# Optimization experiments

Hardware: AMD Instinct MI355X
Metric: run time of the kernel (lower is better)

The kernel has to match this reference:

```python
import jax, jax.numpy as jnp
import numpy as np

GAMMA = 1.0


def setup_inputs() -> dict:
    key = jax.random.key(0)
    kx, ky = jax.random.split(key)
    x = jax.random.normal(kx, (8192, 128), dtype=jnp.float32)
    y = jax.random.normal(ky, (8192, 128), dtype=jnp.float32)
    return {"x": x, "y": y}


def reference(x, y):
    # RBF kernel K[i,j] = exp(-gamma * ||x_i - y_j||^2)
    x2 = jnp.sum(x * x, axis=1)              # [N]
    y2 = jnp.sum(y * y, axis=1)              # [M]
    xy = jnp.einsum('nd,md->nm', x, y)       # [N, M] GEMM
    sq = x2[:, None] + y2[None, :] - 2.0 * xy
    sq = jnp.maximum(sq, 0.0)                # guard tiny negatives from cancellation
    return jnp.exp(-GAMMA * sq)
```

## Files before the change

### kernel.cpp

```cpp
#include <hip/hip_runtime.h>
#include <hip/hip_bf16.h>

typedef __bf16 bf16x8 __attribute__((ext_vector_type(8)));
typedef float f32x4 __attribute__((ext_vector_type(4)));
typedef unsigned short us4 __attribute__((ext_vector_type(4)));

__device__ __forceinline__ unsigned short f2bf(float f) {
    unsigned u = __float_as_uint(f);
    u += 0x7fffu + ((u >> 16) & 1u);
    return (unsigned short)(u >> 16);
}

__global__ __launch_bounds__(256)
void rbf_prep(const float* __restrict__ X, const float* __restrict__ Y,
              unsigned short* __restrict__ Xb, unsigned short* __restrict__ Yb,
              float* __restrict__ x2, float* __restrict__ y2) {
    const int b = blockIdx.x;
    const float* src = (b < 128) ? X : Y;
    unsigned short* db = (b < 128) ? Xb : Yb;
    float* dn = (b < 128) ? x2 : y2;
    const int r0 = (b & 127) * 64;
    const int t = threadIdx.x;
    const f32x4* s4 = (const f32x4*)(src + (size_t)r0 * 128);
#pragma unroll
    for (int i = 0; i < 8; ++i) {
        int idx = i * 256 + t;
        int r = idx >> 5, c4 = idx & 31;
        f32x4 v = s4[idx];
        us4 o;
        o.x = f2bf(v[0]); o.y = f2bf(v[1]); o.z = f2bf(v[2]); o.w = f2bf(v[3]);
        int pc = (c4 >> 1) ^ (r & 7);
        *(us4*)&db[(size_t)(r0 + r) * 128 + pc * 8 + (c4 & 1) * 4] = o;
    }
    if (t < 64) {
        const f32x4* row = (const f32x4*)(src + (size_t)(r0 + t) * 128);
        float s = 0.f;
#pragma unroll
        for (int c = 0; c < 32; ++c) {
            f32x4 v = row[c];
            s += v[0] * v[0] + v[1] * v[1] + v[2] * v[2] + v[3] * v[3];
        }
        dn[r0 + t] = s;
    }
}

__global__ __launch_bounds__(256, 2)
void rbf_main(const unsigned short* __restrict__ Xb, const unsigned short* __restrict__ Yb,
              const float* __restrict__ x2, const float* __restrict__ y2,
              float* __restrict__ O, int ldo) {
    __shared__ __align__(16) unsigned short Ab[16384];
    __shared__ __align__(16) unsigned short Bb[16384];
    const int t = threadIdx.x, l = t & 63, w = t >> 6;
    const int row0 = blockIdx.x * 128, col0 = blockIdx.y * 128;

    const char* gA = (const char*)(Xb + (size_t)row0 * 128);
    const char* gB = (const char*)(Yb + (size_t)col0 * 128);
#pragma unroll
    for (int j = 0; j < 8; ++j) {
        int base = (w * 8 + j) * 1024;
        __builtin_amdgcn_global_load_lds(
            (const __attribute__((address_space(1))) void*)(gA + base + l * 16),
            (__attribute__((address_space(3))) void*)((char*)Ab + base), 16, 0, 0);
        __builtin_amdgcn_global_load_lds(
            (const __attribute__((address_space(1))) void*)(gB + base + l * 16),
            (__attribute__((address_space(3))) void*)((char*)Bb + base), 16, 0, 0);
    }

    const int lr = l & 15, q = l >> 4;
    const int wr = (w >> 1) * 64, wc = (w & 1) * 64;

    f32x4 x2v[4]; float y2v[4];
#pragma unroll
    for (int m = 0; m < 4; ++m) x2v[m] = *(const f32x4*)&x2[row0 + wr + m * 16 + q * 4];
#pragma unroll
    for (int n = 0; n < 4; ++n) y2v[n] = y2[col0 + wc + n * 16 + lr];

    __syncthreads();

    f32x4 acc[4][4] = {};
#pragma unroll
    for (int k = 0; k < 4; ++k) {
        bf16x8 af[4], bv[4];
#pragma unroll
        for (int m = 0; m < 4; ++m) {
            int R = wr + m * 16 + lr;
            af[m] = *(const bf16x8*)((const char*)Ab + R * 256 + (((k << 2) + q) ^ (R & 7)) * 16);
        }
#pragma unroll
        for (int n = 0; n < 4; ++n) {
            int R = wc + n * 16 + lr;
            bv[n] = *(const bf16x8*)((const char*)Bb + R * 256 + (((k << 2) + q) ^ (R & 7)) * 16);
        }
#pragma unroll
        for (int m = 0; m < 4; ++m)
#pragma unroll
            for (int n = 0; n < 4; ++n)
                acc[m][n] = __builtin_amdgcn_mfma_f32_16x16x32_bf16(af[m], bv[n], acc[m][n], 0, 0, 0);
    }

#pragma unroll
    for (int m = 0; m < 4; ++m) {
        int rbase = row0 + wr + m * 16 + q * 4;
#pragma unroll
        for (int n = 0; n < 4; ++n) {
            float* op = &O[(size_t)rbase * ldo + col0 + wc + n * 16 + lr];
            float yv = y2v[n];
#pragma unroll
            for (int i = 0; i < 4; ++i) {
                float sq = x2v[m][i] + yv - 2.0f * acc[m][n][i];
                sq = fmaxf(sq, 0.f);
                __builtin_nontemporal_store(__expf(-sq), op);
                op += ldo;
            }
        }
    }
}

extern "C" void kernel_launch(void* const* d_in, const int* in_sizes, int n_in,
                              void* d_out, int out_size, void* d_ws, size_t ws_size,
                              hipStream_t stream) {
    const float* X = (const float*)d_in[0];
    const float* Y = (const float*)d_in[1];
    float* O = (float*)d_out;
    const int N = in_sizes[0] / 128;
    const int M = in_sizes[1] / 128;
    unsigned short* Xb = (unsigned short*)d_ws;
    unsigned short* Yb = Xb + (size_t)N * 128;
    float* x2 = (float*)(Yb + (size_t)M * 128);
    float* y2 = x2 + N;
    rbf_prep<<<dim3((N + M) / 64), 256, 0, stream>>>(X, Y, Xb, Yb, x2, y2);
    rbf_main<<<dim3(N / 128, M / 128), 256, 0, stream>>>(Xb, Yb, x2, y2, O, M);
}
```

Baseline: 314.2 us.

## Stage output tile through swizzled LDS for coalesced float4 global stores

```diff
diff --git a/kernel.cpp b/kernel.cpp
--- a/kernel.cpp
+++ b/kernel.cpp
@@ -48,8 +48,11 @@
 void rbf_main(const unsigned short* __restrict__ Xb, const unsigned short* __restrict__ Yb,
               const float* __restrict__ x2, const float* __restrict__ y2,
               float* __restrict__ O, int ldo) {
-    __shared__ __align__(16) unsigned short Ab[16384];
-    __shared__ __align__(16) unsigned short Bb[16384];
+    __shared__ __align__(16) char smem[65536];
+    unsigned short* Ab = (unsigned short*)smem;
+    unsigned short* Bb = (unsigned short*)(smem + 32768);
+    float*          Ol = (float*)smem;
+
     const int t = threadIdx.x, l = t & 63, w = t >> 6;
     const int row0 = blockIdx.x * 128, col0 = blockIdx.y * 128;
 
@@ -60,10 +63,10 @@
         int base = (w * 8 + j) * 1024;
         __builtin_amdgcn_global_load_lds(
             (const __attribute__((address_space(1))) void*)(gA + base + l * 16),
-            (__attribute__((address_space(3))) void*)((char*)Ab + base), 16, 0, 0);
+            (__attribute__((address_space(3))) void*)(smem + base), 16, 0, 0);
         __builtin_amdgcn_global_load_lds(
             (const __attribute__((address_space(1))) void*)(gB + base + l * 16),
-            (__attribute__((address_space(3))) void*)((char*)Bb + base), 16, 0, 0);
+            (__attribute__((address_space(3))) void*)(smem + 32768 + base), 16, 0, 0);
     }
 
     const int lr = l & 15, q = l >> 4;
@@ -98,21 +101,34 @@
                 acc[m][n] = __builtin_amdgcn_mfma_f32_16x16x32_bf16(af[m], bv[n], acc[m][n], 0, 0, 0);
     }
 
+    __syncthreads();
+
 #pragma unroll
     for (int m = 0; m < 4; ++m) {
-        int rbase = row0 + wr + m * 16 + q * 4;
+        int rloc = wr + m * 16 + q * 4;
 #pragma unroll
         for (int n = 0; n < 4; ++n) {
-            float* op = &O[(size_t)rbase * ldo + col0 + wc + n * 16 + lr];
+            int col = wc + n * 16 + lr;
+            int lc = col >> 2;
             float yv = y2v[n];
 #pragma unroll
             for (int i = 0; i < 4; ++i) {
-                float sq = x2v[m][i] + yv - 2.0f * acc[m][n][i];
-                sq = fmaxf(sq, 0.f);
-                __builtin_nontemporal_store(__expf(-sq), op);
-                op += ldo;
+                int row = rloc + i;
+                float sq = fmaxf(x2v[m][i] + yv - 2.0f * acc[m][n][i], 0.f);
+                int pc = (lc & 24) | ((lc ^ row) & 7);
+                Ol[row * 128 + pc * 4 + (col & 3)] = __expf(-sq);
             }
         }
+    }
+    __syncthreads();
+
+#pragma unroll
+    for (int i = 0; i < 16; ++i) {
+        int idx = i * 256 + t;
+        int r = idx >> 5, lcc = idx & 31;
+        int pc = (lcc & 24) | ((lcc ^ r) & 7);
+        f32x4 v = *(const f32x4*)((const char*)Ol + r * 512 + pc * 16);
+        *(float4*)&O[(size_t)(row0 + r) * ldo + col0 + lcc * 4] = *(float4*)&v;
     }
 }
 
```

Measured after the change: 286.2 us. 1.1x faster.
